# Optimization experiments

Measured on AMD Instinct MI355X. Metric: run time of the kernel, lower is better.

The kernel has to match this reference:

```python
import jax, jax.numpy as jnp
import numpy as np

N, E = 50000, 800000
IN, C, H, EDIM = 128, 16, 8, 8  # in_channels, out_channels per head, heads, edge_dim
NEG_SLOPE = 0.2


def setup_inputs() -> dict:
    key = jax.random.key(0)
    ks = jax.random.split(key, 10)
    g = 1.0 / np.sqrt(IN)
    inp = {
        "x": jax.random.normal(ks[0], (N, IN), dtype=jnp.float32),
        "edge_index": jax.random.randint(ks[1], (2, E), 0, N, dtype=jnp.int64),
        "edge_attr": jax.random.normal(ks[2], (E, EDIM), dtype=jnp.float32),
        # GATv2Conv params (share_weights=False): lin_l, lin_r with bias, lin_edge no bias
        "W_l": jax.random.normal(ks[3], (IN, H * C), dtype=jnp.float32) * g,
        "b_l": jnp.zeros((H * C,), dtype=jnp.float32),
        "W_r": jax.random.normal(ks[4], (IN, H * C), dtype=jnp.float32) * g,
        "b_r": jnp.zeros((H * C,), dtype=jnp.float32),
        "W_e": jax.random.normal(ks[5], (EDIM, H * C), dtype=jnp.float32) * (1.0 / np.sqrt(EDIM)),
        "att": jax.random.normal(ks[6], (H, C), dtype=jnp.float32) * (1.0 / np.sqrt(C)),
        "bias": jnp.zeros((H * C,), dtype=jnp.float32),
    }
    return inp


def _gatv2_forward(x, edge_index, edge_attr, W_l, b_l, W_r, b_r, W_e, att, bias):
    n = x.shape[0]
    x_l = (x @ W_l + b_l).reshape(n, H, C)  # source transform
    x_r = (x @ W_r + b_r).reshape(n, H, C)  # target transform

    # add self-loops; edge_attr fill_value='mean' (PyG GATv2Conv default)
    loop = jnp.arange(n, dtype=edge_index.dtype)
    src = jnp.concatenate([edge_index[0], loop])
    dst = jnp.concatenate([edge_index[1], loop])
    loop_attr = jnp.broadcast_to(edge_attr.mean(axis=0, keepdims=True), (n, EDIM))
    e_attr = jnp.concatenate([edge_attr, loop_attr], axis=0)  # [E+N, EDIM]

    e_emb = (e_attr @ W_e).reshape(-1, H, C)  # [E+N, H, C]
    m = x_l[src] + x_r[dst] + e_emb          # gather per edge
    m = jax.nn.leaky_relu(m, NEG_SLOPE)
    logit = jnp.einsum("ehc,hc->eh", m, att)  # [E+N, H]

    # destination-grouped (scatter) softmax
    seg_max = jax.ops.segment_max(logit, dst, num_segments=n)
    expd = jnp.exp(logit - seg_max[dst])
    seg_sum = jax.ops.segment_sum(expd, dst, num_segments=n)
    alpha = expd / (seg_sum[dst] + 1e-16)     # [E+N, H]

    msg = alpha[:, :, None] * x_l[src]        # [E+N, H, C]
    out = jax.ops.segment_sum(msg, dst, num_segments=n)  # [N, H, C]
    return out.reshape(n, H * C) + bias       # concat heads + bias


def reference(x, edge_index, edge_attr, W_l, b_l, W_r, b_r, W_e, att, bias):
    return _gatv2_forward(x, edge_index, edge_attr, W_l, b_l, W_r, b_r, W_e, att, bias)
```

## Files before the change

### kernel.cpp

```cpp
#include <hip/hip_runtime.h>

#define NHEAD 8
#define CH    16
#define HC    128
#define INC   128
#define EDIM  8
#define NEG   0.2f

typedef _Float16 h8 __attribute__((ext_vector_type(8)));
typedef _Float16 h2 __attribute__((ext_vector_type(2)));
typedef float    f4 __attribute__((ext_vector_type(4)));

__device__ __forceinline__ float dot2(h2 a, h2 b, float c) {
#if __has_builtin(__builtin_amdgcn_fdot2)
    return __builtin_amdgcn_fdot2(a, b, c, false);
#else
    return c + (float)a[0] * (float)b[0] + (float)a[1] * (float)b[1];
#endif
}

__global__ void k_packW(const float* __restrict__ Wl, const float* __restrict__ Wr,
                        const float* __restrict__ We, const float* __restrict__ att,
                        _Float16* __restrict__ packed,
                        _Float16* __restrict__ We16, _Float16* __restrict__ att16) {
    int id = blockIdx.x * blockDim.x + threadIdx.x;
    int l  = id & 63;
    int kb = (id >> 6) & 3;
    int t  = id >> 8;
    int col = t * 16 + (l & 15);
    const float* W = (col < HC) ? Wl : Wr;
    int c = col & 127;
    int kbase = kb * 32 + (l >> 4) * 8;
    _Float16* dst = packed + (size_t)id * 8;
    #pragma unroll
    for (int j = 0; j < 8; ++j) dst[j] = (_Float16)W[(size_t)(kbase + j) * HC + c];
    if (id < 1024) We16[id] = (_Float16)We[id];
    if (id < 128)  att16[id] = (_Float16)att[id];
}

__global__ __launch_bounds__(256) void k_phase1(
        const float* __restrict__ x, const _Float16* __restrict__ packed,
        const float* __restrict__ bl, const float* __restrict__ br,
        _Float16* __restrict__ xh,
        const int* __restrict__ ei, const float* __restrict__ ea,
        int* __restrict__ cnt, int* __restrict__ rank, float* __restrict__ attr_sum,
        int N, int E, int gemmBlocks) {
    __shared__ _Float16 st[16][264];
    __shared__ float red[4][8];

    if ((int)blockIdx.x < gemmBlocks) {
        int nb0 = blockIdx.x * 64;
        int w  = threadIdx.x >> 6;
        int l  = threadIdx.x & 63;

        const h8* pk = (const h8*)packed;
        h8 bfrag[4][4];
        #pragma unroll
        for (int t4 = 0; t4 < 4; ++t4)
            #pragma unroll
            for (int kb = 0; kb < 4; ++kb)
                bfrag[t4][kb] = pk[(size_t)(((w * 4 + t4) * 4 + kb) * 64 + l)];

        float bv[4];
        int cl = l & 15;
        #pragma unroll
        for (int t4 = 0; t4 < 4; ++t4) {
            int col = w * 64 + t4 * 16 + cl;
            bv[t4] = (col < HC) ? bl[col] : br[col - HC];
        }

        int g = l >> 4;
        int r0 = g * 4;
        for (int mt = 0; mt < 4; ++mt) {
            int m0 = nb0 + mt * 16;
            if (m0 >= N) break;
            int row = m0 + cl; if (row >= N) row = N - 1;
            const float* xp = x + (size_t)row * INC + g * 8;
            h8 afrag[4];
            #pragma unroll
            for (int kb = 0; kb < 4; ++kb) {
                float4 u = *(const float4*)(xp + kb * 32);
                float4 v = *(const float4*)(xp + kb * 32 + 4);
                h8 a;
                a[0] = (_Float16)u.x; a[1] = (_Float16)u.y; a[2] = (_Float16)u.z; a[3] = (_Float16)u.w;
                a[4] = (_Float16)v.x; a[5] = (_Float16)v.y; a[6] = (_Float16)v.z; a[7] = (_Float16)v.w;
                afrag[kb] = a;
            }
            f4 acc[4];
            #pragma unroll
            for (int t4 = 0; t4 < 4; ++t4) { f4 z = {0.f, 0.f, 0.f, 0.f}; acc[t4] = z; }
            #pragma unroll
            for (int kb = 0; kb < 4; ++kb)
                #pragma unroll
                for (int t4 = 0; t4 < 4; ++t4)
                    acc[t4] = __builtin_amdgcn_mfma_f32_16x16x32_f16(afrag[kb], bfrag[t4][kb], acc[t4], 0, 0, 0);
            #pragma unroll
            for (int t4 = 0; t4 < 4; ++t4) {
                int col = w * 64 + t4 * 16 + cl;
                #pragma unroll
                for (int j = 0; j < 4; ++j)
                    st[r0 + j][col] = (_Float16)(acc[t4][j] + bv[t4]);
            }
            __syncthreads();
            #pragma unroll
            for (int q = 0; q < 2; ++q) {
                int cch = threadIdx.x + 256 * q;
                int r = cch >> 5, ch = (cch & 31) * 8;
                int node = m0 + r;
                if (node < N) *(h8*)(xh + (size_t)node * 256 + ch) = *(const h8*)&st[r][ch];
            }
            __syncthreads();
        }
    } else {
        int t = (blockIdx.x - gemmBlocks) * 256 + threadIdx.x;
        float av[8] = {0.f, 0.f, 0.f, 0.f, 0.f, 0.f, 0.f, 0.f};
        if (t < E) {
            rank[t] = atomicAdd(&cnt[ei[E + t]], 1);
            float4 a0 = *(const float4*)(ea + (size_t)t * EDIM);
            float4 a1 = *(const float4*)(ea + (size_t)t * EDIM + 4);
            av[0] = a0.x; av[1] = a0.y; av[2] = a0.z; av[3] = a0.w;
            av[4] = a1.x; av[5] = a1.y; av[6] = a1.z; av[7] = a1.w;
        }
        #pragma unroll
        for (int m = 1; m < 64; m <<= 1) {
            #pragma unroll
            for (int k = 0; k < 8; ++k) av[k] += __shfl_xor(av[k], m);
        }
        int lane = threadIdx.x & 63, wid = threadIdx.x >> 6;
        if (lane == 0) {
            #pragma unroll
            for (int k = 0; k < 8; ++k) red[wid][k] = av[k];
        }
        __syncthreads();
        if (threadIdx.x < 8) {
            float s = red[0][threadIdx.x] + red[1][threadIdx.x] + red[2][threadIdx.x] + red[3][threadIdx.x];
            atomicAdd(&attr_sum[threadIdx.x], s);
        }
    }
}

__global__ void k_scan1(const int* __restrict__ cnt, int* __restrict__ off,
                        int* __restrict__ bsum, int N,
                        const float* __restrict__ attr_sum, const float* __restrict__ We,
                        _Float16* __restrict__ loop16, float invE) {
    __shared__ int wpre[16];
    int i = blockIdx.x * 1024 + threadIdx.x;
    int lane = threadIdx.x & 63, wid = threadIdx.x >> 6;
    int v = (i < N) ? cnt[i] : 0;
    int s = v;
    #pragma unroll
    for (int d = 1; d < 64; d <<= 1) {
        int t = __shfl_up(s, d);
        if (lane >= d) s += t;
    }
    if (lane == 63) wpre[wid] = s;
    __syncthreads();
    if (threadIdx.x == 0) {
        int run = 0;
        #pragma unroll
        for (int q = 0; q < 16; ++q) { int t = wpre[q]; wpre[q] = run; run += t; }
        bsum[blockIdx.x] = run;
    }
    __syncthreads();
    if (i <= N) off[i] = wpre[wid] + s - v;

    if (blockIdx.x == 0 && threadIdx.x < HC) {
        int j = threadIdx.x;
        float acc = 0.f;
        #pragma unroll
        for (int d = 0; d < EDIM; ++d) acc += attr_sum[d] * invE * We[d * HC + j];
        loop16[j] = (_Float16)acc;
    }
}

__global__ void k_scatter(const int* __restrict__ ei, const float* __restrict__ ea,
                          const int* __restrict__ off, const int* __restrict__ bsum,
                          const int* __restrict__ rank,
                          int* __restrict__ esrc, h8* __restrict__ eac, int E, int nb) {
    int lane = threadIdx.x & 63;
    int bv = (lane < nb) ? bsum[lane] : 0;
    int s = bv;
    #pragma unroll
    for (int d = 1; d < 64; d <<= 1) {
        int t = __shfl_up(s, d);
        if (lane >= d) s += t;
    }
    s -= bv;

    int t = blockIdx.x * blockDim.x + threadIdx.x;
    if (t >= E) return;
    int dst = ei[E + t];
    int pos = off[dst] + __shfl(s, dst >> 10) + rank[t];
    esrc[pos] = ei[t];
    float4 a0 = *(const float4*)(ea + (size_t)t * EDIM);
    float4 a1 = *(const float4*)(ea + (size_t)t * EDIM + 4);
    h8 v;
    v[0] = (_Float16)a0.x; v[1] = (_Float16)a0.y; v[2] = (_Float16)a0.z; v[3] = (_Float16)a0.w;
    v[4] = (_Float16)a1.x; v[5] = (_Float16)a1.y; v[6] = (_Float16)a1.z; v[7] = (_Float16)a1.w;
    eac[pos] = v;
}

__global__ __launch_bounds__(256) void k_gather(
        const int* __restrict__ esrc, const h8* __restrict__ eac,
        const _Float16* __restrict__ We16, const _Float16* __restrict__ att16,
        const _Float16* __restrict__ xh, const _Float16* __restrict__ loop16,
        const float* __restrict__ bias,
        const int* __restrict__ off, const int* __restrict__ bsum,
        float* __restrict__ out, int N, int nb) {
    int wid = (blockIdx.x * blockDim.x + threadIdx.x) >> 6;
    int lane = threadIdx.x & 63;
    int dst0 = wid * 2;
    if (dst0 >= N) return;
    int qid = lane >> 4;
    int l   = lane & 15;
    int c0  = l * 8;

    int bv = (lane < nb) ? bsum[lane] : 0;
    int sx = bv;
    #pragma unroll
    for (int d = 1; d < 64; d <<= 1) {
        int t = __shfl_up(sx, d);
        if (lane >= d) sx += t;
    }
    sx -= bv;

    h8 we8[EDIM];
    #pragma unroll
    for (int d = 0; d < EDIM; ++d) we8[d] = *(const h8*)(We16 + d * HC + c0);
    h8 av8 = *(const h8*)(att16 + c0);
    h2 att2[4];
    #pragma unroll
    for (int k = 0; k < 4; ++k) { att2[k][0] = av8[2 * k]; att2[k][1] = av8[2 * k + 1]; }
    h8 lp8 = *(const h8*)(loop16 + c0);
    const h8 z8 = {};
    h8 ng8;
    #pragma unroll
    for (int k = 0; k < 8; ++k) ng8[k] = (_Float16)NEG;

    for (int rep = 0; rep < 2; ++rep) {
        int dst = dst0 + rep;
        if (dst >= N) break;
        dst = __builtin_amdgcn_readfirstlane(dst);

        h8 xr8 = *(const h8*)(xh + (size_t)dst * 256 + HC + c0);

        float accv[8] = {0.f, 0.f, 0.f, 0.f, 0.f, 0.f, 0.f, 0.f};
        float segw = 0.f;

        auto TAIL = [&](h8 m8, h8 x8, bool valid) {
            h8 mp = __builtin_elementwise_max(m8, z8);
            h8 mn = __builtin_elementwise_min(m8, z8);
            m8 = mp + mn * ng8;
            float p = 0.f;
            #pragma unroll
            for (int k = 0; k < 4; ++k) {
                h2 mm; mm[0] = m8[2 * k]; mm[1] = m8[2 * k + 1];
                p = dot2(mm, att2[k], p);
            }
            p += __shfl_xor(p, 1);
            float w = valid ? __expf(p) : 0.f;
            segw += w;
            #pragma unroll
            for (int k = 0; k < 8; ++k) accv[k] += w * (float)x8[k];
        };

        {
            h8 x8 = *(const h8*)(xh + (size_t)dst * 256 + c0);
            TAIL(x8 + xr8 + lp8, x8, qid == 0);
        }

        int q0 = dst >> 10, q1 = (dst + 1) >> 10;
        int beg = off[dst] + __shfl(sx, q0);
        int end = off[dst + 1] + __shfl(sx, q1);
        if (beg < end) {
            int last = end - 1;
            int j = beg + qid; if (j > last) j = last;
            int s0 = esrc[j];
            h8 a0 = eac[j];
            h8 x0 = *(const h8*)(xh + (size_t)s0 * 256 + c0);
            for (int i = beg; i < end; i += 4) {
                int jn = i + 4 + qid; if (jn > last) jn = last;
                int sn = esrc[jn];
                h8 an = eac[jn];
                h8 xn = *(const h8*)(xh + (size_t)sn * 256 + c0);
                h8 m8 = x0 + xr8;
                #pragma unroll
                for (int d = 0; d < EDIM; ++d) {
                    h8 ad = {a0[d], a0[d], a0[d], a0[d], a0[d], a0[d], a0[d], a0[d]};
                    m8 += ad * we8[d];
                }
                TAIL(m8, x0, (i + qid) < end);
                a0 = an; x0 = xn;
            }
        }

        segw += __shfl_xor(segw, 16); segw += __shfl_xor(segw, 32);
        #pragma unroll
        for (int k = 0; k < 8; ++k) {
            accv[k] += __shfl_xor(accv[k], 16);
            accv[k] += __shfl_xor(accv[k], 32);
        }

        if (qid == 0) {
            float inv = 1.f / (segw + 1e-16f);
            f4 b0 = *(const f4*)(bias + c0), b1 = *(const f4*)(bias + c0 + 4);
            f4 o0, o1;
            o0[0] = accv[0] * inv + b0[0]; o0[1] = accv[1] * inv + b0[1];
            o0[2] = accv[2] * inv + b0[2]; o0[3] = accv[3] * inv + b0[3];
            o1[0] = accv[4] * inv + b1[0]; o1[1] = accv[5] * inv + b1[1];
            o1[2] = accv[6] * inv + b1[2]; o1[3] = accv[7] * inv + b1[3];
            *(f4*)(out + (size_t)dst * HC + c0)     = o0;
            *(f4*)(out + (size_t)dst * HC + c0 + 4) = o1;
        }
    }
}

extern "C" void kernel_launch(void* const* d_in, const int* in_sizes, int n_in,
                              void* d_out, int out_size, void* d_ws, size_t ws_size,
                              hipStream_t stream) {
    int N = in_sizes[0] / INC;
    int E = in_sizes[1] / 2;
    const float* x    = (const float*)d_in[0];
    const int*   ei   = (const int*)d_in[1];
    const float* ea   = (const float*)d_in[2];
    const float* Wl   = (const float*)d_in[3];
    const float* bl   = (const float*)d_in[4];
    const float* Wr   = (const float*)d_in[5];
    const float* br   = (const float*)d_in[6];
    const float* We   = (const float*)d_in[7];
    const float* att  = (const float*)d_in[8];
    const float* bias = (const float*)d_in[9];
    float* out = (float*)d_out;

    _Float16* xh      = (_Float16*)d_ws;
    h8*       eac     = (h8*)(xh + (size_t)N * 256);
    float* attr_sum   = (float*)(eac + E);
    int*   cnt        = (int*)(attr_sum + 8);
    _Float16* loop16  = (_Float16*)(cnt + N);
    _Float16* packed  = loop16 + 128;
    _Float16* We16    = packed + 32768;
    _Float16* att16   = We16 + 1024;
    int*   off        = (int*)(att16 + 128);
    int*   rank       = off + (N + 2);
    int*   esrc       = rank + E;
    int*   bsum       = esrc + E;

    hipMemsetAsync(attr_sum, 0, (8 + (size_t)N) * sizeof(float), stream);

    k_packW<<<16, 256, 0, stream>>>(Wl, Wr, We, att, packed, We16, att16);

    int gemmBlocks = (N + 63) / 64;
    int histBlocks = (E + 255) / 256;
    k_phase1<<<gemmBlocks + histBlocks, 256, 0, stream>>>(x, packed, bl, br, xh,
                                                          ei, ea, cnt, rank, attr_sum,
                                                          N, E, gemmBlocks);

    int nb = (N + 1 + 1023) / 1024;
    k_scan1<<<nb, 1024, 0, stream>>>(cnt, off, bsum, N, attr_sum, We, loop16, 1.0f / (float)E);

    k_scatter<<<histBlocks, 256, 0, stream>>>(ei, ea, off, bsum, rank, esrc, eac, E, nb);

    int waves = (N + 1) / 2;
    k_gather<<<(waves * 64 + 255) / 256, 256, 0, stream>>>(esrc, eac, We16, att16, xh, loop16,
                                                           bias, off, bsum, out, N, nb);
}
```

Before: 168.0 us.

## Reorder stages to overlap GEMM with edge scatter and use one node per wave

```diff
diff --git a/kernel.cpp b/kernel.cpp
--- a/kernel.cpp
+++ b/kernel.cpp
@@ -19,34 +19,100 @@
 #endif
 }
 
-__global__ void k_packW(const float* __restrict__ Wl, const float* __restrict__ Wr,
-                        const float* __restrict__ We, const float* __restrict__ att,
-                        _Float16* __restrict__ packed,
-                        _Float16* __restrict__ We16, _Float16* __restrict__ att16) {
-    int id = blockIdx.x * blockDim.x + threadIdx.x;
-    int l  = id & 63;
-    int kb = (id >> 6) & 3;
-    int t  = id >> 8;
-    int col = t * 16 + (l & 15);
-    const float* W = (col < HC) ? Wl : Wr;
-    int c = col & 127;
-    int kbase = kb * 32 + (l >> 4) * 8;
-    _Float16* dst = packed + (size_t)id * 8;
-    #pragma unroll
-    for (int j = 0; j < 8; ++j) dst[j] = (_Float16)W[(size_t)(kbase + j) * HC + c];
-    if (id < 1024) We16[id] = (_Float16)We[id];
-    if (id < 128)  att16[id] = (_Float16)att[id];
-}
-
-__global__ __launch_bounds__(256) void k_phase1(
+__global__ __launch_bounds__(256) void k_histpack(
+        const float* __restrict__ Wl, const float* __restrict__ Wr,
+        const float* __restrict__ We, const float* __restrict__ att,
+        _Float16* __restrict__ packed, _Float16* __restrict__ We16, _Float16* __restrict__ att16,
+        const int* __restrict__ ei, const float* __restrict__ ea,
+        int* __restrict__ cnt, int* __restrict__ rank, float* __restrict__ attr_sum,
+        int E) {
+    __shared__ float red[4][8];
+    if ((int)blockIdx.x < 16) {
+        int id = blockIdx.x * 256 + threadIdx.x;
+        int l  = id & 63;
+        int kb = (id >> 6) & 3;
+        int t  = id >> 8;
+        int col = t * 16 + (l & 15);
+        const float* W = (col < HC) ? Wl : Wr;
+        int c = col & 127;
+        int kbase = kb * 32 + (l >> 4) * 8;
+        _Float16* dst = packed + (size_t)id * 8;
+        #pragma unroll
+        for (int j = 0; j < 8; ++j) dst[j] = (_Float16)W[(size_t)(kbase + j) * HC + c];
+        if (id < 1024) We16[id] = (_Float16)We[id];
+        if (id < 128)  att16[id] = (_Float16)att[id];
+    } else {
+        int t = (blockIdx.x - 16) * 256 + threadIdx.x;
+        float av[8] = {0.f, 0.f, 0.f, 0.f, 0.f, 0.f, 0.f, 0.f};
+        if (t < E) {
+            rank[t] = atomicAdd(&cnt[ei[E + t]], 1);
+            float4 a0 = *(const float4*)(ea + (size_t)t * EDIM);
+            float4 a1 = *(const float4*)(ea + (size_t)t * EDIM + 4);
+            av[0] = a0.x; av[1] = a0.y; av[2] = a0.z; av[3] = a0.w;
+            av[4] = a1.x; av[5] = a1.y; av[6] = a1.z; av[7] = a1.w;
+        }
+        #pragma unroll
+        for (int m = 1; m < 64; m <<= 1) {
+            #pragma unroll
+            for (int k = 0; k < 8; ++k) av[k] += __shfl_xor(av[k], m);
+        }
+        int lane = threadIdx.x & 63, wid = threadIdx.x >> 6;
+        if (lane == 0) {
+            #pragma unroll
+            for (int k = 0; k < 8; ++k) red[wid][k] = av[k];
+        }
+        __syncthreads();
+        if (threadIdx.x < 8) {
+            float s = red[0][threadIdx.x] + red[1][threadIdx.x] + red[2][threadIdx.x] + red[3][threadIdx.x];
+            atomicAdd(&attr_sum[threadIdx.x], s);
+        }
+    }
+}
+
+__global__ void k_scan1(const int* __restrict__ cnt, int* __restrict__ off,
+                        int* __restrict__ bsum, int N,
+                        const float* __restrict__ attr_sum, const float* __restrict__ We,
+                        _Float16* __restrict__ loop16, float invE) {
+    __shared__ int wpre[16];
+    int i = blockIdx.x * 1024 + threadIdx.x;
+    int lane = threadIdx.x & 63, wid = threadIdx.x >> 6;
+    int v = (i < N) ? cnt[i] : 0;
+    int s = v;
+    #pragma unroll
+    for (int d = 1; d < 64; d <<= 1) {
+        int t = __shfl_up(s, d);
+        if (lane >= d) s += t;
+    }
+    if (lane == 63) wpre[wid] = s;
+    __syncthreads();
+    if (threadIdx.x == 0) {
+        int run = 0;
+        #pragma unroll
+        for (int q = 0; q < 16; ++q) { int t = wpre[q]; wpre[q] = run; run += t; }
+        bsum[blockIdx.x] = run;
+    }
+    __syncthreads();
+    if (i <= N) off[i] = wpre[wid] + s - v;
+
+    if (blockIdx.x == 0 && threadIdx.x < HC) {
+        int j = threadIdx.x;
+        float acc = 0.f;
+        #pragma unroll
+        for (int d = 0; d < EDIM; ++d) acc += attr_sum[d] * invE * We[d * HC + j];
+        loop16[j] = (_Float16)acc;
+    }
+}
+
+__global__ __launch_bounds__(256) void k_phase2(
         const float* __restrict__ x, const _Float16* __restrict__ packed,
         const float* __restrict__ bl, const float* __restrict__ br,
         _Float16* __restrict__ xh,
         const int* __restrict__ ei, const float* __restrict__ ea,
-        int* __restrict__ cnt, int* __restrict__ rank, float* __restrict__ attr_sum,
-        int N, int E, int gemmBlocks) {
+        const int* __restrict__ off, const int* __restrict__ bsum,
+        const int* __restrict__ rank,
+        int* __restrict__ esrc, h8* __restrict__ eac,
+        int N, int E, int gemmBlocks, int nb) {
     __shared__ _Float16 st[16][264];
-    __shared__ float red[4][8];
 
     if ((int)blockIdx.x < gemmBlocks) {
         int nb0 = blockIdx.x * 64;
@@ -112,92 +178,28 @@
             __syncthreads();
         }
     } else {
+        int lane = threadIdx.x & 63;
+        int bv = (lane < nb) ? bsum[lane] : 0;
+        int s = bv;
+        #pragma unroll
+        for (int d = 1; d < 64; d <<= 1) {
+            int t = __shfl_up(s, d);
+            if (lane >= d) s += t;
+        }
+        s -= bv;
+
         int t = (blockIdx.x - gemmBlocks) * 256 + threadIdx.x;
-        float av[8] = {0.f, 0.f, 0.f, 0.f, 0.f, 0.f, 0.f, 0.f};
-        if (t < E) {
-            rank[t] = atomicAdd(&cnt[ei[E + t]], 1);
-            float4 a0 = *(const float4*)(ea + (size_t)t * EDIM);
-            float4 a1 = *(const float4*)(ea + (size_t)t * EDIM + 4);
-            av[0] = a0.x; av[1] = a0.y; av[2] = a0.z; av[3] = a0.w;
-            av[4] = a1.x; av[5] = a1.y; av[6] = a1.z; av[7] = a1.w;
-        }
-        #pragma unroll
-        for (int m = 1; m < 64; m <<= 1) {
-            #pragma unroll
-            for (int k = 0; k < 8; ++k) av[k] += __shfl_xor(av[k], m);
-        }
-        int lane = threadIdx.x & 63, wid = threadIdx.x >> 6;
-        if (lane == 0) {
-            #pragma unroll
-            for (int k = 0; k < 8; ++k) red[wid][k] = av[k];
-        }
-        __syncthreads();
-        if (threadIdx.x < 8) {
-            float s = red[0][threadIdx.x] + red[1][threadIdx.x] + red[2][threadIdx.x] + red[3][threadIdx.x];
-            atomicAdd(&attr_sum[threadIdx.x], s);
-        }
-    }
-}
-
-__global__ void k_scan1(const int* __restrict__ cnt, int* __restrict__ off,
-                        int* __restrict__ bsum, int N,
-                        const float* __restrict__ attr_sum, const float* __restrict__ We,
-                        _Float16* __restrict__ loop16, float invE) {
-    __shared__ int wpre[16];
-    int i = blockIdx.x * 1024 + threadIdx.x;
-    int lane = threadIdx.x & 63, wid = threadIdx.x >> 6;
-    int v = (i < N) ? cnt[i] : 0;
-    int s = v;
-    #pragma unroll
-    for (int d = 1; d < 64; d <<= 1) {
-        int t = __shfl_up(s, d);
-        if (lane >= d) s += t;
-    }
-    if (lane == 63) wpre[wid] = s;
-    __syncthreads();
-    if (threadIdx.x == 0) {
-        int run = 0;
-        #pragma unroll
-        for (int q = 0; q < 16; ++q) { int t = wpre[q]; wpre[q] = run; run += t; }
-        bsum[blockIdx.x] = run;
-    }
-    __syncthreads();
-    if (i <= N) off[i] = wpre[wid] + s - v;
-
-    if (blockIdx.x == 0 && threadIdx.x < HC) {
-        int j = threadIdx.x;
-        float acc = 0.f;
-        #pragma unroll
-        for (int d = 0; d < EDIM; ++d) acc += attr_sum[d] * invE * We[d * HC + j];
-        loop16[j] = (_Float16)acc;
-    }
-}
-
-__global__ void k_scatter(const int* __restrict__ ei, const float* __restrict__ ea,
-                          const int* __restrict__ off, const int* __restrict__ bsum,
-                          const int* __restrict__ rank,
-                          int* __restrict__ esrc, h8* __restrict__ eac, int E, int nb) {
-    int lane = threadIdx.x & 63;
-    int bv = (lane < nb) ? bsum[lane] : 0;
-    int s = bv;
-    #pragma unroll
-    for (int d = 1; d < 64; d <<= 1) {
-        int t = __shfl_up(s, d);
-        if (lane >= d) s += t;
-    }
-    s -= bv;
-
-    int t = blockIdx.x * blockDim.x + threadIdx.x;
-    if (t >= E) return;
-    int dst = ei[E + t];
-    int pos = off[dst] + __shfl(s, dst >> 10) + rank[t];
-    esrc[pos] = ei[t];
-    float4 a0 = *(const float4*)(ea + (size_t)t * EDIM);
-    float4 a1 = *(const float4*)(ea + (size_t)t * EDIM + 4);
-    h8 v;
-    v[0] = (_Float16)a0.x; v[1] = (_Float16)a0.y; v[2] = (_Float16)a0.z; v[3] = (_Float16)a0.w;
-    v[4] = (_Float16)a1.x; v[5] = (_Float16)a1.y; v[6] = (_Float16)a1.z; v[7] = (_Float16)a1.w;
-    eac[pos] = v;
+        if (t >= E) return;
+        int dst = ei[E + t];
+        int pos = off[dst] + __shfl(s, dst >> 10) + rank[t];
+        esrc[pos] = ei[t];
+        float4 a0 = *(const float4*)(ea + (size_t)t * EDIM);
+        float4 a1 = *(const float4*)(ea + (size_t)t * EDIM + 4);
+        h8 v;
+        v[0] = (_Float16)a0.x; v[1] = (_Float16)a0.y; v[2] = (_Float16)a0.z; v[3] = (_Float16)a0.w;
+        v[4] = (_Float16)a1.x; v[5] = (_Float16)a1.y; v[6] = (_Float16)a1.z; v[7] = (_Float16)a1.w;
+        eac[pos] = v;
+    }
 }
 
 __global__ __launch_bounds__(256) void k_gather(
@@ -207,10 +209,10 @@
         const float* __restrict__ bias,
         const int* __restrict__ off, const int* __restrict__ bsum,
         float* __restrict__ out, int N, int nb) {
-    int wid = (blockIdx.x * blockDim.x + threadIdx.x) >> 6;
+    int wave = (blockIdx.x * blockDim.x + threadIdx.x) >> 6;
     int lane = threadIdx.x & 63;
-    int dst0 = wid * 2;
-    if (dst0 >= N) return;
+    if (wave >= N) return;
+    int dst = __builtin_amdgcn_readfirstlane(wave);
     int qid = lane >> 4;
     int l   = lane & 15;
     int c0  = l * 8;
@@ -237,81 +239,75 @@
     #pragma unroll
     for (int k = 0; k < 8; ++k) ng8[k] = (_Float16)NEG;
 
-    for (int rep = 0; rep < 2; ++rep) {
-        int dst = dst0 + rep;
-        if (dst >= N) break;
-        dst = __builtin_amdgcn_readfirstlane(dst);
-
-        h8 xr8 = *(const h8*)(xh + (size_t)dst * 256 + HC + c0);
-
-        float accv[8] = {0.f, 0.f, 0.f, 0.f, 0.f, 0.f, 0.f, 0.f};
-        float segw = 0.f;
-
-        auto TAIL = [&](h8 m8, h8 x8, bool valid) {
-            h8 mp = __builtin_elementwise_max(m8, z8);
-            h8 mn = __builtin_elementwise_min(m8, z8);
-            m8 = mp + mn * ng8;
-            float p = 0.f;
-            #pragma unroll
-            for (int k = 0; k < 4; ++k) {
-                h2 mm; mm[0] = m8[2 * k]; mm[1] = m8[2 * k + 1];
-                p = dot2(mm, att2[k], p);
+    h8 xr8 = *(const h8*)(xh + (size_t)dst * 256 + HC + c0);
+
+    float accv[8] = {0.f, 0.f, 0.f, 0.f, 0.f, 0.f, 0.f, 0.f};
+    float segw = 0.f;
+
+    auto TAIL = [&](h8 m8, h8 x8, bool valid) {
+        h8 mp = __builtin_elementwise_max(m8, z8);
+        h8 mn = __builtin_elementwise_min(m8, z8);
+        m8 = mp + mn * ng8;
+        float p = 0.f;
+        #pragma unroll
+        for (int k = 0; k < 4; ++k) {
+            h2 mm; mm[0] = m8[2 * k]; mm[1] = m8[2 * k + 1];
+            p = dot2(mm, att2[k], p);
+        }
+        p += __shfl_xor(p, 1);
+        float w = valid ? __expf(p) : 0.f;
+        segw += w;
+        #pragma unroll
+        for (int k = 0; k < 8; ++k) accv[k] += w * (float)x8[k];
+    };
+
+    {
+        h8 x8 = *(const h8*)(xh + (size_t)dst * 256 + c0);
+        TAIL(x8 + xr8 + lp8, x8, qid == 0);
+    }
+
+    int q0 = dst >> 10, q1 = (dst + 1) >> 10;
+    int beg = off[dst] + __shfl(sx, q0);
+    int end = off[dst + 1] + __shfl(sx, q1);
+    if (beg < end) {
+        int last = end - 1;
+        int j = beg + qid; if (j > last) j = last;
+        int s0 = esrc[j];
+        h8 a0 = eac[j];
+        h8 x0 = *(const h8*)(xh + (size_t)s0 * 256 + c0);
+        for (int i = beg; i < end; i += 4) {
+            int jn = i + 4 + qid; if (jn > last) jn = last;
+            int sn = esrc[jn];
+            h8 an = eac[jn];
+            h8 xn = *(const h8*)(xh + (size_t)sn * 256 + c0);
+            h8 m8 = x0 + xr8;
+            #pragma unroll
+            for (int d = 0; d < EDIM; ++d) {
+                h8 ad = {a0[d], a0[d], a0[d], a0[d], a0[d], a0[d], a0[d], a0[d]};
+                m8 += ad * we8[d];
             }
-            p += __shfl_xor(p, 1);
-            float w = valid ? __expf(p) : 0.f;
-            segw += w;
-            #pragma unroll
-            for (int k = 0; k < 8; ++k) accv[k] += w * (float)x8[k];
-        };
-
-        {
-            h8 x8 = *(const h8*)(xh + (size_t)dst * 256 + c0);
-            TAIL(x8 + xr8 + lp8, x8, qid == 0);
-        }
-
-        int q0 = dst >> 10, q1 = (dst + 1) >> 10;
-        int beg = off[dst] + __shfl(sx, q0);
-        int end = off[dst + 1] + __shfl(sx, q1);
-        if (beg < end) {
-            int last = end - 1;
-            int j = beg + qid; if (j > last) j = last;
-            int s0 = esrc[j];
-            h8 a0 = eac[j];
-            h8 x0 = *(const h8*)(xh + (size_t)s0 * 256 + c0);
-            for (int i = beg; i < end; i += 4) {
-                int jn = i + 4 + qid; if (jn > last) jn = last;
-                int sn = esrc[jn];
-                h8 an = eac[jn];
-                h8 xn = *(const h8*)(xh + (size_t)sn * 256 + c0);
-                h8 m8 = x0 + xr8;
-                #pragma unroll
-                for (int d = 0; d < EDIM; ++d) {
-                    h8 ad = {a0[d], a0[d], a0[d], a0[d], a0[d], a0[d], a0[d], a0[d]};
-                    m8 += ad * we8[d];
-                }
-                TAIL(m8, x0, (i + qid) < end);
-                a0 = an; x0 = xn;
-            }
-        }
-
-        segw += __shfl_xor(segw, 16); segw += __shfl_xor(segw, 32);
-        #pragma unroll
-        for (int k = 0; k < 8; ++k) {
-            accv[k] += __shfl_xor(accv[k], 16);
-            accv[k] += __shfl_xor(accv[k], 32);
-        }
-
-        if (qid == 0) {
-            float inv = 1.f / (segw + 1e-16f);
-            f4 b0 = *(const f4*)(bias + c0), b1 = *(const f4*)(bias + c0 + 4);
-            f4 o0, o1;
-            o0[0] = accv[0] * inv + b0[0]; o0[1] = accv[1] * inv + b0[1];
-            o0[2] = accv[2] * inv + b0[2]; o0[3] = accv[3] * inv + b0[3];
-            o1[0] = accv[4] * inv + b1[0]; o1[1] = accv[5] * inv + b1[1];
-            o1[2] = accv[6] * inv + b1[2]; o1[3] = accv[7] * inv + b1[3];
-            *(f4*)(out + (size_t)dst * HC + c0)     = o0;
-            *(f4*)(out + (size_t)dst * HC + c0 + 4) = o1;
-        }
+            TAIL(m8, x0, (i + qid) < end);
+            a0 = an; x0 = xn;
+        }
+    }
+
+    segw += __shfl_xor(segw, 16); segw += __shfl_xor(segw, 32);
+    #pragma unroll
+    for (int k = 0; k < 8; ++k) {
+        accv[k] += __shfl_xor(accv[k], 16);
+        accv[k] += __shfl_xor(accv[k], 32);
+    }
+
+    if (qid == 0) {
+        float inv = 1.f / (segw + 1e-16f);
+        f4 b0 = *(const f4*)(bias + c0), b1 = *(const f4*)(bias + c0 + 4);
+        f4 o0, o1;
+        o0[0] = accv[0] * inv + b0[0]; o0[1] = accv[1] * inv + b0[1];
+        o0[2] = accv[2] * inv + b0[2]; o0[3] = accv[3] * inv + b0[3];
+        o1[0] = accv[4] * inv + b1[0]; o1[1] = accv[5] * inv + b1[1];
+        o1[2] = accv[6] * inv + b1[2]; o1[3] = accv[7] * inv + b1[3];
+        *(f4*)(out + (size_t)dst * HC + c0)     = o0;
+        *(f4*)(out + (size_t)dst * HC + c0 + 4) = o1;
     }
 }
 
@@ -347,20 +343,18 @@
 
     hipMemsetAsync(attr_sum, 0, (8 + (size_t)N) * sizeof(float), stream);
 
-    k_packW<<<16, 256, 0, stream>>>(Wl, Wr, We, att, packed, We16, att16);
-
-    int gemmBlocks = (N + 63) / 64;
     int histBlocks = (E + 255) / 256;
-    k_phase1<<<gemmBlocks + histBlocks, 256, 0, stream>>>(x, packed, bl, br, xh,
-                                                          ei, ea, cnt, rank, attr_sum,
-                                                          N, E, gemmBlocks);
+    k_histpack<<<16 + histBlocks, 256, 0, stream>>>(Wl, Wr, We, att, packed, We16, att16,
+                                                    ei, ea, cnt, rank, attr_sum, E);
 
     int nb = (N + 1 + 1023) / 1024;
     k_scan1<<<nb, 1024, 0, stream>>>(cnt, off, bsum, N, attr_sum, We, loop16, 1.0f / (float)E);
 
-    k_scatter<<<histBlocks, 256, 0, stream>>>(ei, ea, off, bsum, rank, esrc, eac, E, nb);
-
-    int waves = (N + 1) / 2;
-    k_gather<<<(waves * 64 + 255) / 256, 256, 0, stream>>>(esrc, eac, We16, att16, xh, loop16,
-                                                           bias, off, bsum, out, N, nb);
-}
+    int gemmBlocks = (N + 63) / 64;
+    k_phase2<<<gemmBlocks + histBlocks, 256, 0, stream>>>(x, packed, bl, br, xh,
+                                                          ei, ea, off, bsum, rank,
+                                                          esrc, eac, N, E, gemmBlocks, nb);
+
+    k_gather<<<((size_t)N * 64 + 255) / 256, 256, 0, stream>>>(esrc, eac, We16, att16, xh, loop16,
+                                                               bias, off, bsum, out, N, nb);
+}
```

Result: no change. 166.0 us (-1.2%).
